# Optimization experiments

Hardware: AMD Instinct MI355X
Metric: run time of the kernel (lower is better)

## Reference

```python
import jax, jax.numpy as jnp
import numpy as np

B, N, D, H = 16, 256, 512, 8
DK = D // H          # 64
DIM_G = 64           # trigonometric geometry embedding dim
WAVE_LEN = 1000.0


def box_relational_embedding(boxes):
    # boxes: [B, N, 4] = (x_min, y_min, x_max, y_max)
    x_min, y_min, x_max, y_max = jnp.split(boxes, 4, axis=-1)  # each [B,N,1]
    cx = ((x_min + x_max) * 0.5)[..., 0]   # [B,N]
    cy = ((y_min + y_max) * 0.5)[..., 0]
    w = (x_max - x_min + 1.0)[..., 0]
    h = (y_max - y_min + 1.0)[..., 0]
    # pairwise deltas, normalized by the *row* box size (as in the torch code)
    dx = jnp.log(jnp.clip(jnp.abs((cx[:, :, None] - cx[:, None, :]) / w[:, :, None]), 1e-3))
    dy = jnp.log(jnp.clip(jnp.abs((cy[:, :, None] - cy[:, None, :]) / h[:, :, None]), 1e-3))
    dw = jnp.log(w[:, :, None] / w[:, None, :])
    dh = jnp.log(h[:, :, None] / h[:, None, :])
    pos = jnp.stack([dx, dy, dw, dh], axis=-1)  # [B,N,N,4]
    # trig embedding: freq per (dim_g/8) channels
    feat_range = jnp.arange(DIM_G // 8, dtype=pos.dtype) / (DIM_G / 8.0)
    dim_mat = 1.0 / jnp.power(WAVE_LEN, feat_range)               # [8]
    mul = (100.0 * pos)[..., None] * dim_mat                      # [B,N,N,4,8]
    mul = mul.reshape(mul.shape[:3] + (-1,))                      # [B,N,N,32]
    return jnp.concatenate([jnp.sin(mul), jnp.cos(mul)], axis=-1)  # [B,N,N,64]


def setup_inputs() -> dict:
    key = jax.random.key(0)
    ks = jax.random.split(key, 16)
    inp = {
        'input_query': jax.random.normal(ks[0], (B, N, D), jnp.float32),
        'input_key': jax.random.normal(ks[1], (B, N, D), jnp.float32),
        'input_value': jax.random.normal(ks[2], (B, N, D), jnp.float32),
    }
    # valid boxes: x_max > x_min, y_max > y_min
    xm = jax.random.uniform(ks[3], (B, N, 1)) * 800.0
    ym = jax.random.uniform(ks[4], (B, N, 1)) * 800.0
    bw = jax.random.uniform(ks[5], (B, N, 1)) * 120.0 + 5.0
    bh = jax.random.uniform(ks[6], (B, N, 1)) * 120.0 + 5.0
    inp['input_box'] = jnp.concatenate([xm, ym, xm + bw, ym + bh], axis=-1)
    s = 1.0 / np.sqrt(D)
    inp['Wq'] = jax.random.normal(ks[7], (D, D), jnp.float32) * s
    inp['bq'] = jnp.zeros((D,), jnp.float32)
    inp['Wk'] = jax.random.normal(ks[8], (D, D), jnp.float32) * s
    inp['bk'] = jnp.zeros((D,), jnp.float32)
    inp['Wv'] = jax.random.normal(ks[9], (D, D), jnp.float32) * s
    inp['bv'] = jnp.zeros((D,), jnp.float32)
    inp['Wo'] = jax.random.normal(ks[10], (D, D), jnp.float32) * s
    inp['bo'] = jnp.zeros((D,), jnp.float32)
    inp['Wg'] = jax.random.normal(ks[11], (H, DIM_G), jnp.float32) * (1.0 / np.sqrt(DIM_G))
    inp['bg'] = jnp.zeros((H,), jnp.float32)
    return inp


def reference(input_query, input_key, input_value, input_box,
              Wq, bq, Wk, bk, Wv, bv, Wo, bo, Wg, bg):
    nb = input_query.shape[0]
    geo = box_relational_embedding(input_box)                     # [B,N,N,64]
    wg = jax.nn.relu(jnp.einsum('bijg,hg->bhij', geo, Wg) + bg[None, :, None, None])
    def proj(x, W, b):
        return (x @ W + b).reshape(nb, -1, H, DK).transpose(0, 2, 1, 3)  # [B,H,N,dk]
    q = proj(input_query, Wq, bq)
    k = proj(input_key, Wk, bk)
    v = proj(input_value, Wv, bv)
    scores = jnp.einsum('bhid,bhjd->bhij', q, k) / np.sqrt(DK)    # [B,H,N,N]
    w_mn = jax.nn.softmax(jnp.log(jnp.clip(wg, 1e-6)) + scores, axis=-1)
    out = jnp.einsum('bhij,bhjd->bhid', w_mn, v)                  # [B,H,N,dk]
    out = out.transpose(0, 2, 1, 3).reshape(nb, -1, H * DK)       # [B,N,D]
    return out @ Wo + bo
```

## Files before the change

kernel.cpp:

```cpp
#include <hip/hip_runtime.h>
#include <hip/hip_bf16.h>

#define B_ 16
#define N_ 256
#define D_ 512
#define H_ 8
#define DK_ 64

typedef unsigned short u16;
typedef __attribute__((ext_vector_type(8))) short bf16x8;
typedef __attribute__((ext_vector_type(4))) float f32x4;

__device__ __forceinline__ float bf2f(u16 u) {
    union { unsigned int i; float f; } v;
    v.i = ((unsigned int)u) << 16;
    return v.f;
}
__device__ __forceinline__ u16 f2bf(float f) {
    union { float f; unsigned int i; } v;
    v.f = f;
    unsigned int x = v.i;
    unsigned int r = (x >> 16) & 1u;
    x += 0x7fffu + r;
    return (u16)(x >> 16);
}

__global__ __launch_bounds__(256) void k_prep(const float* __restrict__ box,
                                              const float* __restrict__ Wg,
                                              const float* __restrict__ bg,
                                              u16* __restrict__ Sg,
                                              const float* __restrict__ W0,
                                              const float* __restrict__ W1,
                                              const float* __restrict__ W2,
                                              const float* __restrict__ W3,
                                              u16* __restrict__ Wt,
                                              const float* __restrict__ X0,
                                              const float* __restrict__ X1,
                                              const float* __restrict__ X2,
                                              u16* __restrict__ Xb) {
    const int tid = threadIdx.x;
    const int bid = blockIdx.x;
    if (bid < 4096) {
        __shared__ float sWg[8][64];
        __shared__ float sbg[8];
        if (tid < 8) sbg[tid] = bg[tid];
        { int e = tid; sWg[e >> 6][e & 63] = Wg[e];
          e = tid + 256; sWg[e >> 6][e & 63] = Wg[e]; }
        const int bi = bid, b = bi >> 8;
        float4 bxi = *(const float4*)&box[(size_t)bi * 4];
        float4 bxj = *(const float4*)&box[(size_t)(b * N_ + tid) * 4];
        __syncthreads();
        float cxi = (bxi.x + bxi.z) * 0.5f, cyi = (bxi.y + bxi.w) * 0.5f;
        float wi = bxi.z - bxi.x + 1.0f, hi = bxi.w - bxi.y + 1.0f;
        float cxj = (bxj.x + bxj.z) * 0.5f, cyj = (bxj.y + bxj.w) * 0.5f;
        float wj = bxj.z - bxj.x + 1.0f, hj = bxj.w - bxj.y + 1.0f;
        float pos[4];
        pos[0] = __logf(fmaxf(fabsf((cxi - cxj) / wi), 1e-3f));
        pos[1] = __logf(fmaxf(fabsf((cyi - cyj) / hi), 1e-3f));
        pos[2] = __logf(wi / wj);
        pos[3] = __logf(hi / hj);
        const float dm[8] = {1.0f, 0.42169650342858224f, 0.1778279410038923f,
                             0.07498942093324559f, 0.03162277660168379f,
                             0.013335214321633241f, 0.005623413251903491f,
                             0.0023713737056616554f};
        const float inv2pi = 0.15915494309189535f;
        float acc[8];
#pragma unroll
        for (int h = 0; h < 8; ++h) acc[h] = sbg[h];
#pragma unroll
        for (int t = 0; t < 4; ++t) {
            float base = 100.0f * pos[t];
#pragma unroll
            for (int f = 0; f < 8; ++f) {
                float rev = base * dm[f] * inv2pi;
                rev = rev - floorf(rev);
                float sn = __builtin_amdgcn_sinf(rev);
                float cs = __builtin_amdgcn_cosf(rev);
                int idx = t * 8 + f;
#pragma unroll
                for (int h = 0; h < 8; ++h)
                    acc[h] += sWg[h][idx] * sn + sWg[h][idx + 32] * cs;
            }
        }
        const int i = bi & 255;
#pragma unroll
        for (int h = 0; h < 8; ++h)
            Sg[(((size_t)(b * H_ + h) * N_) + i) * N_ + tid] =
                f2bf(__logf(fmaxf(acc[h], 1e-6f)));
    } else if (bid < 5120) {
        __shared__ float tt[32][33];
        int t = bid - 4096;
        int z = t >> 8, yb = (t >> 4) & 15, xb = t & 15;
        const float* W = (z == 0) ? W0 : (z == 1) ? W1 : (z == 2) ? W2 : W3;
        u16* dst = Wt + (size_t)z * 262144;
        const int kb = yb * 32, nb = xb * 32;
#pragma unroll
        for (int r = 0; r < 4; ++r) {
            int p = r * 256 + tid;
            tt[p >> 5][p & 31] = W[(size_t)(kb + (p >> 5)) * 512 + nb + (p & 31)];
        }
        __syncthreads();
#pragma unroll
        for (int r = 0; r < 4; ++r) {
            int p = r * 256 + tid;
            dst[(size_t)(nb + (p >> 5)) * 512 + kb + (p & 31)] = f2bf(tt[p & 31][p >> 5]);
        }
    } else {
        int t = bid - 5120;
        int z = t >> 10, x = t & 1023;
        const float* X = (z == 0) ? X0 : (z == 1) ? X1 : X2;
        u16* dst = Xb + (size_t)z * 2097152;
        int base = (x * 256 + tid) * 8;
        float4 a = *(const float4*)&X[base];
        float4 b = *(const float4*)&X[base + 4];
        ushort4 oa, ob;
        oa.x = f2bf(a.x); oa.y = f2bf(a.y); oa.z = f2bf(a.z); oa.w = f2bf(a.w);
        ob.x = f2bf(b.x); ob.y = f2bf(b.y); ob.z = f2bf(b.z); ob.w = f2bf(b.w);
        *(ushort4*)&dst[base] = oa;
        *(ushort4*)&dst[base + 4] = ob;
    }
}

__global__ __launch_bounds__(256) void k_gemm_qkv(const u16* __restrict__ Xb,
                                                  const u16* __restrict__ Wtb,
                                                  const float* __restrict__ bq,
                                                  const float* __restrict__ bk,
                                                  const float* __restrict__ bv,
                                                  u16* __restrict__ qkv) {
    const int z = blockIdx.z;
    const u16* Ab = Xb + (size_t)z * 2097152;
    const u16* Wt = Wtb + (size_t)z * 262144;
    const float* bias = (z == 0) ? bq : (z == 1) ? bk : bv;
    u16* dst = qkv + (size_t)z * 2097152;

    __shared__ u16 As[2][64][72];
    __shared__ u16 Bs[2][64][72];
    const int tid = threadIdx.x;
    const int m0 = blockIdx.x * 64, n0 = blockIdx.y * 64;
    const int wid = tid >> 6, lane = tid & 63;
    const int wm = (wid & 1) * 32, wn = (wid >> 1) * 32;
    const int lr = lane & 15, lk8 = (lane >> 4) * 8, quad4 = (lane >> 4) * 4;

    f32x4 acc[2][2];
#pragma unroll
    for (int mi = 0; mi < 2; ++mi)
#pragma unroll
        for (int ni = 0; ni < 2; ++ni) acc[mi][ni] = (f32x4){0.f, 0.f, 0.f, 0.f};

    ushort4 ra[4], rb[4];
#pragma unroll
    for (int r = 0; r < 4; ++r) {
        int p = r * 256 + tid, row = p >> 4, c4 = (p & 15) * 4;
        ra[r] = *(const ushort4*)&Ab[(size_t)(m0 + row) * 512 + c4];
        rb[r] = *(const ushort4*)&Wt[(size_t)(n0 + row) * 512 + c4];
    }
#pragma unroll
    for (int r = 0; r < 4; ++r) {
        int p = r * 256 + tid, row = p >> 4, c4 = (p & 15) * 4;
        *(ushort4*)&As[0][row][c4] = ra[r];
        *(ushort4*)&Bs[0][row][c4] = rb[r];
    }
    __syncthreads();
    for (int it = 0; it < 8; ++it) {
        const int cur = it & 1;
        if (it < 7) {
            int k0n = (it + 1) * 64;
#pragma unroll
            for (int r = 0; r < 4; ++r) {
                int p = r * 256 + tid, row = p >> 4, c4 = (p & 15) * 4;
                ra[r] = *(const ushort4*)&Ab[(size_t)(m0 + row) * 512 + k0n + c4];
                rb[r] = *(const ushort4*)&Wt[(size_t)(n0 + row) * 512 + k0n + c4];
            }
        }
#pragma unroll
        for (int ks = 0; ks < 64; ks += 32) {
            bf16x8 af[2], bfx[2];
#pragma unroll
            for (int mi = 0; mi < 2; ++mi)
                af[mi] = *(const bf16x8*)&As[cur][wm + mi * 16 + lr][ks + lk8];
#pragma unroll
            for (int ni = 0; ni < 2; ++ni)
                bfx[ni] = *(const bf16x8*)&Bs[cur][wn + ni * 16 + lr][ks + lk8];
#pragma unroll
            for (int mi = 0; mi < 2; ++mi)
#pragma unroll
                for (int ni = 0; ni < 2; ++ni)
                    acc[mi][ni] = __builtin_amdgcn_mfma_f32_16x16x32_bf16(
                        af[mi], bfx[ni], acc[mi][ni], 0, 0, 0);
        }
        if (it < 7) {
#pragma unroll
            for (int r = 0; r < 4; ++r) {
                int p = r * 256 + tid, row = p >> 4, c4 = (p & 15) * 4;
                *(ushort4*)&As[1 - cur][row][c4] = ra[r];
                *(ushort4*)&Bs[1 - cur][row][c4] = rb[r];
            }
            __syncthreads();
        }
    }
    u16* bounce = &As[0][0][0];
    const float scale = (z == 0) ? 0.125f : 1.0f;
    const int h = n0 >> 6, b = m0 >> 8, rrb = m0 & 255;
    if (z == 2) {
#pragma unroll
        for (int mi = 0; mi < 2; ++mi)
#pragma unroll
            for (int ni = 0; ni < 2; ++ni) {
                int cn = wn + ni * 16 + lr;
                float bb = bias[n0 + cn];
#pragma unroll
                for (int reg = 0; reg < 4; ++reg) {
                    int rm = wm + mi * 16 + quad4 + reg;
                    bounce[cn * 72 + rm] = f2bf(acc[mi][ni][reg] + bb);
                }
            }
        __syncthreads();
#pragma unroll
        for (int r = 0; r < 4; ++r) {
            int p = r * 256 + tid, dn = p >> 4, c4 = (p & 15) * 4;
            *(ushort4*)&dst[(((size_t)(b * H_ + h) * DK_) + dn) * N_ + rrb + c4] =
                *(const ushort4*)&bounce[dn * 72 + c4];
        }
    } else {
#pragma unroll
        for (int mi = 0; mi < 2; ++mi)
#pragma unroll
            for (int ni = 0; ni < 2; ++ni) {
                int cn = wn + ni * 16 + lr;
                float bb = bias[n0 + cn];
#pragma unroll
                for (int reg = 0; reg < 4; ++reg) {
                    int rm = wm + mi * 16 + quad4 + reg;
                    bounce[rm * 72 + cn] = f2bf((acc[mi][ni][reg] + bb) * scale);
                }
            }
        __syncthreads();
#pragma unroll
        for (int r = 0; r < 4; ++r) {
            int p = r * 256 + tid, rm = p >> 4, c4 = (p & 15) * 4;
            *(ushort4*)&dst[(((size_t)(b * H_ + h) * N_) + rrb + rm) * DK_ + c4] =
                *(const ushort4*)&bounce[rm * 72 + c4];
        }
    }
}

__global__ __launch_bounds__(256) void k_gemm_out(const u16* __restrict__ Ab,
                                                  const u16* __restrict__ Wt,
                                                  const float* __restrict__ bias,
                                                  float* __restrict__ outp) {
    __shared__ u16 As[2][64][72];
    __shared__ u16 Bs[2][64][72];
    const int tid = threadIdx.x;
    const int m0 = blockIdx.x * 64, n0 = blockIdx.y * 64;
    const int wid = tid >> 6, lane = tid & 63;
    const int wm = (wid & 1) * 32, wn = (wid >> 1) * 32;
    const int lr = lane & 15, lk8 = (lane >> 4) * 8;
    f32x4 acc[2][2];
#pragma unroll
    for (int mi = 0; mi < 2; ++mi)
#pragma unroll
        for (int ni = 0; ni < 2; ++ni) acc[mi][ni] = (f32x4){0.f, 0.f, 0.f, 0.f};
    ushort4 ra[4], rb[4];
#pragma unroll
    for (int r = 0; r < 4; ++r) {
        int p = r * 256 + tid, row = p >> 4, c4 = (p & 15) * 4;
        ra[r] = *(const ushort4*)&Ab[(size_t)(m0 + row) * 512 + c4];
        rb[r] = *(const ushort4*)&Wt[(size_t)(n0 + row) * 512 + c4];
    }
#pragma unroll
    for (int r = 0; r < 4; ++r) {
        int p = r * 256 + tid, row = p >> 4, c4 = (p & 15) * 4;
        *(ushort4*)&As[0][row][c4] = ra[r];
        *(ushort4*)&Bs[0][row][c4] = rb[r];
    }
    __syncthreads();
    for (int it = 0; it < 8; ++it) {
        const int cur = it & 1;
        if (it < 7) {
            int k0n = (it + 1) * 64;
#pragma unroll
            for (int r = 0; r < 4; ++r) {
                int p = r * 256 + tid, row = p >> 4, c4 = (p & 15) * 4;
                ra[r] = *(const ushort4*)&Ab[(size_t)(m0 + row) * 512 + k0n + c4];
                rb[r] = *(const ushort4*)&Wt[(size_t)(n0 + row) * 512 + k0n + c4];
            }
        }
#pragma unroll
        for (int ks = 0; ks < 64; ks += 32) {
            bf16x8 af[2], bfx[2];
#pragma unroll
            for (int mi = 0; mi < 2; ++mi)
                af[mi] = *(const bf16x8*)&As[cur][wm + mi * 16 + lr][ks + lk8];
#pragma unroll
            for (int ni = 0; ni < 2; ++ni)
                bfx[ni] = *(const bf16x8*)&Bs[cur][wn + ni * 16 + lr][ks + lk8];
#pragma unroll
            for (int mi = 0; mi < 2; ++mi)
#pragma unroll
                for (int ni = 0; ni < 2; ++ni)
                    acc[mi][ni] = __builtin_amdgcn_mfma_f32_16x16x32_bf16(
                        af[mi], bfx[ni], acc[mi][ni], 0, 0, 0);
        }
        if (it < 7) {
#pragma unroll
            for (int r = 0; r < 4; ++r) {
                int p = r * 256 + tid, row = p >> 4, c4 = (p & 15) * 4;
                *(ushort4*)&As[1 - cur][row][c4] = ra[r];
                *(ushort4*)&Bs[1 - cur][row][c4] = rb[r];
            }
            __syncthreads();
        }
    }
#pragma unroll
    for (int mi = 0; mi < 2; ++mi)
#pragma unroll
        for (int ni = 0; ni < 2; ++ni) {
            int col = n0 + wn + ni * 16 + lr;
            float bb = bias[col];
#pragma unroll
            for (int reg = 0; reg < 4; ++reg) {
                int m = m0 + wm + mi * 16 + (lane >> 4) * 4 + reg;
                outp[(size_t)m * 512 + col] = acc[mi][ni][reg] + bb;
            }
        }
}

__global__ __launch_bounds__(256) void k_attn(const u16* __restrict__ qh,
                                              const u16* __restrict__ kh,
                                              const u16* __restrict__ vhT,
                                              const u16* __restrict__ Sg,
                                              u16* __restrict__ attnb) {
    __shared__ __align__(16) unsigned char smem[63488];
    u16* sQ = (u16*)smem;
    u16* sP = (u16*)(smem + 9216);
    u16* sK = (u16*)(smem + 43008);
    u16* sVt = (u16*)(smem + 43008);
    float* sRedM = (float*)(smem + 61440);
    float* sRedS = (float*)(smem + 62464);

    const int tid = threadIdx.x;
    const int bh = blockIdx.x;
    const int i0 = blockIdx.y * 64;
    const int b = bh >> 3, h = bh & 7;
    const int wid = tid >> 6, lane = tid & 63;
    const int lr = lane & 15, lk8 = (lane >> 4) * 8, quad4 = (lane >> 4) * 4;

#pragma unroll
    for (int r = 0; r < 4; ++r) {
        int p = r * 256 + tid, i = p >> 4, d0 = (p & 15) * 4;
        *(ushort4*)&sQ[i * 72 + d0] =
            *(const ushort4*)&qh[((size_t)bh * N_ + i0 + i) * DK_ + d0];
    }
#pragma unroll
    for (int r = 0; r < 16; ++r) {
        int p = r * 256 + tid, row = p >> 6, jc = (p & 63) * 4;
        *(ushort4*)&sP[row * 264 + jc] =
            *(const ushort4*)&Sg[(((size_t)bh * N_) + i0 + row) * N_ + jc];
    }
#pragma unroll
    for (int r = 0; r < 8; ++r) {
        int p = r * 256 + tid, j = p >> 4, d0 = (p & 15) * 4;
        *(ushort4*)&sK[j * 72 + d0] =
            *(const ushort4*)&kh[((size_t)bh * N_ + j) * DK_ + d0];
    }
    __syncthreads();

    ushort4 kpre[8];
#pragma unroll
    for (int r = 0; r < 8; ++r) {
        int p = r * 256 + tid, j = p >> 4, d0 = (p & 15) * 4;
        kpre[r] = *(const ushort4*)&kh[((size_t)bh * N_ + 128 + j) * DK_ + d0];
    }
    f32x4 acc[2][4][2];
#pragma unroll
    for (int c = 0; c < 2; ++c)
#pragma unroll
        for (int mi = 0; mi < 4; ++mi)
#pragma unroll
            for (int ni = 0; ni < 2; ++ni) acc[c][mi][ni] = (f32x4){0.f, 0.f, 0.f, 0.f};
#pragma unroll
    for (int ks = 0; ks < 64; ks += 32) {
        bf16x8 af[4], bfx[2];
#pragma unroll
        for (int mi = 0; mi < 4; ++mi)
            af[mi] = *(const bf16x8*)&sQ[(mi * 16 + lr) * 72 + ks + lk8];
#pragma unroll
        for (int ni = 0; ni < 2; ++ni)
            bfx[ni] = *(const bf16x8*)&sK[(wid * 32 + ni * 16 + lr) * 72 + ks + lk8];
#pragma unroll
        for (int mi = 0; mi < 4; ++mi)
#pragma unroll
            for (int ni = 0; ni < 2; ++ni)
                acc[0][mi][ni] = __builtin_amdgcn_mfma_f32_16x16x32_bf16(
                    af[mi], bfx[ni], acc[0][mi][ni], 0, 0, 0);
    }
    __syncthreads();
#pragma unroll
    for (int r = 0; r < 8; ++r) {
        int p = r * 256 + tid, j = p >> 4, d0 = (p & 15) * 4;
        *(ushort4*)&sK[j * 72 + d0] = kpre[r];
    }
    __syncthreads();
#pragma unroll
    for (int ks = 0; ks < 64; ks += 32) {
        bf16x8 af[4], bfx[2];
#pragma unroll
        for (int mi = 0; mi < 4; ++mi)
            af[mi] = *(const bf16x8*)&sQ[(mi * 16 + lr) * 72 + ks + lk8];
#pragma unroll
        for (int ni = 0; ni < 2; ++ni)
            bfx[ni] = *(const bf16x8*)&sK[(wid * 32 + ni * 16 + lr) * 72 + ks + lk8];
#pragma unroll
        for (int mi = 0; mi < 4; ++mi)
#pragma unroll
            for (int ni = 0; ni < 2; ++ni)
                acc[1][mi][ni] = __builtin_amdgcn_mfma_f32_16x16x32_bf16(
                    af[mi], bfx[ni], acc[1][mi][ni], 0, 0, 0);
    }
    __syncthreads();

#pragma unroll
    for (int r = 0; r < 8; ++r) {
        int p = r * 256 + tid, d = p >> 5, jc = (p & 31) * 4;
        *(ushort4*)&sVt[d * 136 + jc] =
            *(const ushort4*)&vhT[(((size_t)bh * DK_) + d) * N_ + jc];
    }
#pragma unroll
    for (int c = 0; c < 2; ++c)
#pragma unroll
        for (int mi = 0; mi < 4; ++mi)
#pragma unroll
            for (int ni = 0; ni < 2; ++ni) {
                int col = c * 128 + wid * 32 + ni * 16 + lr;
#pragma unroll
                for (int reg = 0; reg < 4; ++reg) {
                    int row = mi * 16 + quad4 + reg;
                    acc[c][mi][ni][reg] += bf2f(sP[row * 264 + col]);
                }
            }
    float mrow[4][4];
#pragma unroll
    for (int mi = 0; mi < 4; ++mi)
#pragma unroll
        for (int reg = 0; reg < 4; ++reg) {
            float m = acc[0][mi][0][reg];
            m = fmaxf(m, acc[0][mi][1][reg]);
            m = fmaxf(m, acc[1][mi][0][reg]);
            m = fmaxf(m, acc[1][mi][1][reg]);
#pragma unroll
            for (int off = 1; off <= 8; off <<= 1) m = fmaxf(m, __shfl_xor(m, off, 64));
            mrow[mi][reg] = m;
        }
    if (lr == 0) {
#pragma unroll
        for (int mi = 0; mi < 4; ++mi)
#pragma unroll
            for (int reg = 0; reg < 4; ++reg)
                sRedM[(mi * 16 + quad4 + reg) * 4 + wid] = mrow[mi][reg];
    }
    __syncthreads();
    float gm[4][4], sl[4][4];
#pragma unroll
    for (int mi = 0; mi < 4; ++mi)
#pragma unroll
        for (int reg = 0; reg < 4; ++reg) {
            float4 mm = *(const float4*)&sRedM[(mi * 16 + quad4 + reg) * 4];
            gm[mi][reg] = fmaxf(fmaxf(mm.x, mm.y), fmaxf(mm.z, mm.w));
            sl[mi][reg] = 0.f;
        }
#pragma unroll
    for (int c = 0; c < 2; ++c)
#pragma unroll
        for (int mi = 0; mi < 4; ++mi)
#pragma unroll
            for (int ni = 0; ni < 2; ++ni)
#pragma unroll
                for (int reg = 0; reg < 4; ++reg) {
                    float e = __expf(acc[c][mi][ni][reg] - gm[mi][reg]);
                    acc[c][mi][ni][reg] = e;
                    sl[mi][reg] += e;
                }
#pragma unroll
    for (int mi = 0; mi < 4; ++mi)
#pragma unroll
        for (int reg = 0; reg < 4; ++reg) {
            float s = sl[mi][reg];
#pragma unroll
            for (int off = 1; off <= 8; off <<= 1) s += __shfl_xor(s, off, 64);
            sl[mi][reg] = s;
        }
    if (lr == 0) {
#pragma unroll
        for (int mi = 0; mi < 4; ++mi)
#pragma unroll
            for (int reg = 0; reg < 4; ++reg)
                sRedS[(mi * 16 + quad4 + reg) * 4 + wid] = sl[mi][reg];
    }
    __syncthreads();
#pragma unroll
    for (int mi = 0; mi < 4; ++mi)
#pragma unroll
        for (int reg = 0; reg < 4; ++reg) {
            float4 ss = *(const float4*)&sRedS[(mi * 16 + quad4 + reg) * 4];
            gm[mi][reg] = 1.0f / (ss.x + ss.y + ss.z + ss.w);
        }
#pragma unroll
    for (int c = 0; c < 2; ++c)
#pragma unroll
        for (int mi = 0; mi < 4; ++mi)
#pragma unroll
            for (int ni = 0; ni < 2; ++ni) {
                int col = c * 128 + wid * 32 + ni * 16 + lr;
#pragma unroll
                for (int reg = 0; reg < 4; ++reg) {
                    int row = mi * 16 + quad4 + reg;
                    sP[row * 264 + col] = f2bf(acc[c][mi][ni][reg] * gm[mi][reg]);
                }
            }
    __syncthreads();

    f32x4 o[4];
#pragma unroll
    for (int mi = 0; mi < 4; ++mi) o[mi] = (f32x4){0.f, 0.f, 0.f, 0.f};
#pragma unroll
    for (int k0 = 0; k0 < 128; k0 += 32) {
        bf16x8 bfx = *(const bf16x8*)&sVt[(wid * 16 + lr) * 136 + k0 + lk8];
#pragma unroll
        for (int mi = 0; mi < 4; ++mi) {
            bf16x8 af = *(const bf16x8*)&sP[(mi * 16 + lr) * 264 + k0 + lk8];
            o[mi] = __builtin_amdgcn_mfma_f32_16x16x32_bf16(af, bfx, o[mi], 0, 0, 0);
        }
    }
    __syncthreads();
#pragma unroll
    for (int r = 0; r < 8; ++r) {
        int p = r * 256 + tid, d = p >> 5, jc = (p & 31) * 4;
        *(ushort4*)&sVt[d * 136 + jc] =
            *(const ushort4*)&vhT[(((size_t)bh * DK_) + d) * N_ + 128 + jc];
    }
    __syncthreads();
#pragma unroll
    for (int k0 = 0; k0 < 128; k0 += 32) {
        bf16x8 bfx = *(const bf16x8*)&sVt[(wid * 16 + lr) * 136 + k0 + lk8];
#pragma unroll
        for (int mi = 0; mi < 4; ++mi) {
            bf16x8 af = *(const bf16x8*)&sP[(mi * 16 + lr) * 264 + 128 + k0 + lk8];
            o[mi] = __builtin_amdgcn_mfma_f32_16x16x32_bf16(af, bfx, o[mi], 0, 0, 0);
        }
    }
#pragma unroll
    for (int mi = 0; mi < 4; ++mi)
#pragma unroll
        for (int reg = 0; reg < 4; ++reg) {
            int row = mi * 16 + quad4 + reg;
            attnb[((size_t)(b * N_ + i0 + row)) * D_ + h * 64 + wid * 16 + lr] =
                f2bf(o[mi][reg]);
        }
}

extern "C" void kernel_launch(void* const* d_in, const int* in_sizes, int n_in,
                              void* d_out, int out_size, void* d_ws, size_t ws_size,
                              hipStream_t stream) {
    const float* Xq = (const float*)d_in[0];
    const float* Xk = (const float*)d_in[1];
    const float* Xv = (const float*)d_in[2];
    const float* box = (const float*)d_in[3];
    const float* Wq = (const float*)d_in[4];
    const float* bq = (const float*)d_in[5];
    const float* Wk = (const float*)d_in[6];
    const float* bk = (const float*)d_in[7];
    const float* Wv = (const float*)d_in[8];
    const float* bv = (const float*)d_in[9];
    const float* Wo = (const float*)d_in[10];
    const float* bo = (const float*)d_in[11];
    const float* Wg = (const float*)d_in[12];
    const float* bg = (const float*)d_in[13];
    float* out = (float*)d_out;

    u16* ws16 = (u16*)d_ws;
    u16* qkv = ws16;
    u16* qh = qkv;
    u16* kh = qkv + 2097152;
    u16* vhT = qkv + 4194304;
    u16* Sg = ws16 + 6291456;
    u16* attnb = ws16 + 14680064;
    u16* Wt = ws16 + 16777216;
    u16* Xb = ws16 + 18874368;

    dim3 blk(256);
    k_prep<<<dim3(8192), blk, 0, stream>>>(box, Wg, bg, Sg, Wq, Wk, Wv, Wo, Wt,
                                           Xq, Xk, Xv, Xb);
    k_gemm_qkv<<<dim3(64, 8, 3), blk, 0, stream>>>(Xb, Wt, bq, bk, bv, qkv);
    k_attn<<<dim3(128, 4), blk, 0, stream>>>(qh, kh, vhT, Sg, attnb);
    k_gemm_out<<<dim3(64, 8), blk, 0, stream>>>(attnb, Wt + 3 * 262144, bo, out);
}
```

Before: 162.8 us.

## Compute geometry head projection with bf16 MFMA and coalesce bias-map stores via LDS

The geometry-weight branch of the prep kernel no longer does a scalar 64x8 FMA reduction per pair. It writes the bf16 sin/cos features to shared memory and computes the 8-head projection with 16x16x32 bf16 MFMA instructions, padding the head dimension to 16. Results are staged through an LDS bounce buffer so each head row is written to global memory as contiguous vector stores. This trades fp32 accuracy in the Wg projection for bf16 inputs and adds extra barriers and shared-memory traffic.

Result: no change. 161.9 us (-0.6%).

```diff
diff --git a/kernel.cpp b/kernel.cpp
--- a/kernel.cpp
+++ b/kernel.cpp
@@ -38,18 +38,17 @@
                                               const float* __restrict__ X1,
                                               const float* __restrict__ X2,
                                               u16* __restrict__ Xb) {
+    __shared__ __align__(16) unsigned char sh[36864];
     const int tid = threadIdx.x;
     const int bid = blockIdx.x;
     if (bid < 4096) {
-        __shared__ float sWg[8][64];
-        __shared__ float sbg[8];
-        if (tid < 8) sbg[tid] = bg[tid];
-        { int e = tid; sWg[e >> 6][e & 63] = Wg[e];
-          e = tid + 256; sWg[e >> 6][e & 63] = Wg[e]; }
-        const int bi = bid, b = bi >> 8;
+        u16* feat = (u16*)sh;
+        const int bi = bid, b = bi >> 8, i = bi & 255;
+        const int wid = tid >> 6, lane = tid & 63;
+        const int lr = lane & 15, lk8 = (lane >> 4) * 8, quad4 = (lane >> 4) * 4;
+
         float4 bxi = *(const float4*)&box[(size_t)bi * 4];
         float4 bxj = *(const float4*)&box[(size_t)(b * N_ + tid) * 4];
-        __syncthreads();
         float cxi = (bxi.x + bxi.z) * 0.5f, cyi = (bxi.y + bxi.w) * 0.5f;
         float wi = bxi.z - bxi.x + 1.0f, hi = bxi.w - bxi.y + 1.0f;
         float cxj = (bxj.x + bxj.z) * 0.5f, cyj = (bxj.y + bxj.w) * 0.5f;
@@ -64,31 +63,85 @@
                              0.013335214321633241f, 0.005623413251903491f,
                              0.0023713737056616554f};
         const float inv2pi = 0.15915494309189535f;
-        float acc[8];
-#pragma unroll
-        for (int h = 0; h < 8; ++h) acc[h] = sbg[h];
 #pragma unroll
         for (int t = 0; t < 4; ++t) {
             float base = 100.0f * pos[t];
+            float sn[8], cs[8];
 #pragma unroll
             for (int f = 0; f < 8; ++f) {
                 float rev = base * dm[f] * inv2pi;
                 rev = rev - floorf(rev);
-                float sn = __builtin_amdgcn_sinf(rev);
-                float cs = __builtin_amdgcn_cosf(rev);
-                int idx = t * 8 + f;
-#pragma unroll
-                for (int h = 0; h < 8; ++h)
-                    acc[h] += sWg[h][idx] * sn + sWg[h][idx + 32] * cs;
-            }
-        }
-        const int i = bi & 255;
-#pragma unroll
-        for (int h = 0; h < 8; ++h)
-            Sg[(((size_t)(b * H_ + h) * N_) + i) * N_ + tid] =
-                f2bf(__logf(fmaxf(acc[h], 1e-6f)));
+                sn[f] = __builtin_amdgcn_sinf(rev);
+                cs[f] = __builtin_amdgcn_cosf(rev);
+            }
+            ushort4 p;
+            p.x = f2bf(sn[0]); p.y = f2bf(sn[1]); p.z = f2bf(sn[2]); p.w = f2bf(sn[3]);
+            *(ushort4*)&feat[tid * 72 + t * 8] = p;
+            p.x = f2bf(sn[4]); p.y = f2bf(sn[5]); p.z = f2bf(sn[6]); p.w = f2bf(sn[7]);
+            *(ushort4*)&feat[tid * 72 + t * 8 + 4] = p;
+            p.x = f2bf(cs[0]); p.y = f2bf(cs[1]); p.z = f2bf(cs[2]); p.w = f2bf(cs[3]);
+            *(ushort4*)&feat[tid * 72 + 32 + t * 8] = p;
+            p.x = f2bf(cs[4]); p.y = f2bf(cs[5]); p.z = f2bf(cs[6]); p.w = f2bf(cs[7]);
+            *(ushort4*)&feat[tid * 72 + 32 + t * 8 + 4] = p;
+        }
+        bf16x8 bw0, bw1;
+        float bgv = 0.f;
+        if (lr < 8) {
+            const float* wrow = &Wg[lr * 64];
+            float4 a0 = *(const float4*)&wrow[lk8];
+            float4 a1 = *(const float4*)&wrow[lk8 + 4];
+            float4 a2 = *(const float4*)&wrow[32 + lk8];
+            float4 a3 = *(const float4*)&wrow[32 + lk8 + 4];
+            bw0[0] = (short)f2bf(a0.x); bw0[1] = (short)f2bf(a0.y);
+            bw0[2] = (short)f2bf(a0.z); bw0[3] = (short)f2bf(a0.w);
+            bw0[4] = (short)f2bf(a1.x); bw0[5] = (short)f2bf(a1.y);
+            bw0[6] = (short)f2bf(a1.z); bw0[7] = (short)f2bf(a1.w);
+            bw1[0] = (short)f2bf(a2.x); bw1[1] = (short)f2bf(a2.y);
+            bw1[2] = (short)f2bf(a2.z); bw1[3] = (short)f2bf(a2.w);
+            bw1[4] = (short)f2bf(a3.x); bw1[5] = (short)f2bf(a3.y);
+            bw1[6] = (short)f2bf(a3.z); bw1[7] = (short)f2bf(a3.w);
+            bgv = bg[lr];
+        } else {
+#pragma unroll
+            for (int e = 0; e < 8; ++e) { bw0[e] = 0; bw1[e] = 0; }
+        }
+        __syncthreads();
+        f32x4 dacc[4];
+#pragma unroll
+        for (int q = 0; q < 4; ++q) {
+            int jt = wid * 4 + q;
+            bf16x8 a0 = *(const bf16x8*)&feat[(jt * 16 + lr) * 72 + lk8];
+            bf16x8 a1 = *(const bf16x8*)&feat[(jt * 16 + lr) * 72 + 32 + lk8];
+            f32x4 z = (f32x4){0.f, 0.f, 0.f, 0.f};
+            z = __builtin_amdgcn_mfma_f32_16x16x32_bf16(a0, bw0, z, 0, 0, 0);
+            z = __builtin_amdgcn_mfma_f32_16x16x32_bf16(a1, bw1, z, 0, 0, 0);
+            dacc[q] = z;
+        }
+        __syncthreads();
+        u16* bounce = (u16*)sh;
+        if (lr < 8) {
+#pragma unroll
+            for (int q = 0; q < 4; ++q) {
+                int jt = wid * 4 + q;
+#pragma unroll
+                for (int reg = 0; reg < 4; ++reg) {
+                    float wg = dacc[q][reg] + bgv;
+                    bounce[lr * 264 + jt * 16 + quad4 + reg] =
+                        f2bf(__logf(fmaxf(wg, 1e-6f)));
+                }
+            }
+        }
+        __syncthreads();
+        {
+            int h = tid >> 5, jb = (tid & 31) * 8;
+            ushort4 v0 = *(const ushort4*)&bounce[h * 264 + jb];
+            ushort4 v1 = *(const ushort4*)&bounce[h * 264 + jb + 4];
+            u16* dstp = &Sg[(((size_t)(b * H_ + h) * N_) + i) * N_ + jb];
+            *(ushort4*)&dstp[0] = v0;
+            *(ushort4*)&dstp[4] = v1;
+        }
     } else if (bid < 5120) {
-        __shared__ float tt[32][33];
+        float (*tt)[33] = (float(*)[33])sh;
         int t = bid - 4096;
         int z = t >> 8, yb = (t >> 4) & 15, xb = t & 15;
         const float* W = (z == 0) ? W0 : (z == 1) ? W1 : (z == 2) ? W2 : W3;
```
